# Kernel tuning notes

Hardware: AMD Instinct MI355X
Metric: run time of the kernel (lower is better)

The kernel has to match this reference:

```python
import jax, jax.numpy as jnp
import numpy as np

NU, NI, D, H, E, NQ = 200000, 100000, 64, 64, 1000000, 100000


def setup_inputs() -> dict:
    key = jax.random.key(0)
    ks = jax.random.split(key, 16)
    s = 0.05
    inp = {
        'user_emb': jax.random.normal(ks[0], (NU, D), jnp.float32) * s,
        'item_emb': jax.random.normal(ks[1], (NI, D), jnp.float32) * s,
        'W1': jax.random.normal(ks[2], (6, D, H), jnp.float32) * s,
        'b1': jnp.zeros((6, H), jnp.float32),
        'W2': jax.random.normal(ks[3], (6, H, H), jnp.float32) * s,
        'b2': jnp.zeros((6, H), jnp.float32),
        'dec_w1': jax.random.normal(ks[4], (2 * H, H), jnp.float32) * s,
        'dec_b1': jnp.zeros((H,), jnp.float32),
        'dec_w2': jax.random.normal(ks[5], (H, 4), jnp.float32) * s,
        'dec_b2': jnp.zeros((4,), jnp.float32),
    }
    for name, k in [('edge_view', ks[6]), ('edge_save', ks[7]), ('edge_buy', ks[8])]:
        src = jax.random.randint(k, (E,), 0, NU, jnp.int64 if jax.config.jax_enable_x64 else jnp.int32)
        dst = jax.random.randint(jax.random.fold_in(k, 1), (E,), 0, NI, src.dtype)
        inp[name] = jnp.stack([src, dst])  # [2, E], row0=user, row1=item
    inp['user_ids'] = jax.random.randint(ks[9], (NQ,), 0, NU, jnp.int32)
    inp['item_ids'] = jax.random.randint(ks[10], (NQ,), 0, NI, jnp.int32)
    return inp


def _gcn_conv(h_src, src, dst, n_src, n_dst, W, b):
    # GCNConv (add_self_loops=False) on a bipartite relation:
    # out[d] = sum_e 1/sqrt(deg_src[src_e]) * 1/sqrt(deg_dst[d]) * (x W)[src_e] + b
    h = h_src @ W  # [n_src, H]
    ones = jnp.ones(src.shape[0], h.dtype)
    deg_s = jax.ops.segment_sum(ones, src, num_segments=n_src)
    deg_d = jax.ops.segment_sum(ones, dst, num_segments=n_dst)
    inv_s = jnp.where(deg_s > 0, jax.lax.rsqrt(jnp.maximum(deg_s, 1.0)), 0.0)
    inv_d = jnp.where(deg_d > 0, jax.lax.rsqrt(jnp.maximum(deg_d, 1.0)), 0.0)
    norm = inv_s[src] * inv_d[dst]  # [E]
    msg = h[src] * norm[:, None]    # [E, H]  (dominant memory traffic)
    return jax.ops.segment_sum(msg, dst, num_segments=n_dst) + b


def _hetero_layer(xu, xi, edges, W, b, aggr):
    # relations 0..2: user->item (view,save,buy); 3..5: item->user (reverses)
    item_outs = jnp.stack([_gcn_conv(xu, e[0], e[1], NU, NI, W[k], b[k])
                           for k, e in enumerate(edges)])
    user_outs = jnp.stack([_gcn_conv(xi, e[1], e[0], NI, NU, W[k + 3], b[k + 3])
                           for k, e in enumerate(edges)])
    if aggr == 'max':
        return user_outs.max(0), item_outs.max(0)
    return user_outs.sum(0), item_outs.sum(0)


def reference(user_emb, item_emb, W1, b1, W2, b2, dec_w1, dec_b1, dec_w2, dec_b2,
              edge_view, edge_save, edge_buy, user_ids, item_ids):
    edges = [edge_view, edge_save, edge_buy]
    xu, xi = _hetero_layer(user_emb, item_emb, edges, W1, b1, 'max')
    xu, xi = jax.nn.relu(xu), jax.nn.relu(xi)
    xu, xi = _hetero_layer(xu, xi, edges, W2, b2, 'sum')
    edge_emb = jnp.concatenate([xu[user_ids], xi[item_ids]], axis=-1)  # [NQ, 2H]
    h = jax.nn.relu(edge_emb @ dec_w1 + dec_b1)  # dropout in eval mode = identity
    return h @ dec_w2 + dec_b2  # [NQ, 4]
```

## Files before the change

kernel.cpp:

```cpp
#include <hip/hip_runtime.h>
#include <hip/hip_fp16.h>
#include <math.h>

#define NUV 200000
#define NIV 100000
#define EV  1000000
#define NQV 100000
#define NC  (3 * NIV + 3 * NUV)

struct alignas(8) H4 { __half2 a, b; };

__global__ __launch_bounds__(256) void k_tohalf(const float* __restrict__ in,
                                                __half* __restrict__ out, int n4) {
    int i = blockIdx.x * 256 + threadIdx.x;
    if (i < n4) {
        float4 v = ((const float4*)in)[i];
        H4 o;
        o.a = __floats2half2_rn(v.x, v.y);
        o.b = __floats2half2_rn(v.z, v.w);
        ((H4*)out)[i] = o;
    }
}

__global__ __launch_bounds__(256) void k_count(const int* __restrict__ su,
                                               const int* __restrict__ di,
                                               int* __restrict__ cnt,
                                               int* __restrict__ rk_i,
                                               int* __restrict__ rk_u, int k) {
    int e = blockIdx.x * 256 + threadIdx.x;
    if (e < EV) {
        rk_i[e] = atomicAdd(&cnt[k * NIV + di[e]], 1);
        rk_u[e] = atomicAdd(&cnt[3 * NIV + k * NUV + su[e]], 1);
    }
}

__global__ __launch_bounds__(256) void k_invf(const int* __restrict__ cnt,
                                              float* __restrict__ invs) {
    int i = blockIdx.x * 256 + threadIdx.x;
    if (i < NC) {
        int c = cnt[i];
        invs[i] = (c > 0) ? (1.0f / sqrtf((float)c)) : 0.0f;
    }
}

__global__ __launch_bounds__(256) void k_scan1(const int* __restrict__ cnt,
                                               int* __restrict__ S,
                                               int* __restrict__ bsum) {
    __shared__ int tmp[256];
    int idx = blockIdx.x * 256 + threadIdx.x;
    int v = (idx < NC) ? cnt[idx] : 0;
    tmp[threadIdx.x] = v;
    __syncthreads();
    for (int off = 1; off < 256; off <<= 1) {
        int t = (threadIdx.x >= off) ? tmp[threadIdx.x - off] : 0;
        __syncthreads();
        tmp[threadIdx.x] += t;
        __syncthreads();
    }
    if (idx < NC) S[idx] = tmp[threadIdx.x] - v;
    if (threadIdx.x == 255) bsum[blockIdx.x] = tmp[255];
}

__global__ __launch_bounds__(64) void k_scan2(int* __restrict__ bsum, int nb) {
    int lane = threadIdx.x;
    int carry = 0;
    for (int base = 0; base < nb; base += 64) {
        int i = base + lane;
        int v = (i < nb) ? bsum[i] : 0;
        int orig = v;
        #pragma unroll
        for (int off = 1; off < 64; off <<= 1) {
            int t = __shfl_up(v, off, 64);
            if (lane >= off) v += t;
        }
        if (i < nb) bsum[i] = carry + v - orig;
        carry += __shfl(v, 63, 64);
    }
}

__global__ __launch_bounds__(256) void k_scan3(int* __restrict__ S,
                                               const int* __restrict__ bsum) {
    int idx = blockIdx.x * 256 + threadIdx.x;
    if (idx < NC) S[idx] += bsum[blockIdx.x];
    if (idx == 0) S[NC] = 6 * EV;
}

__global__ __launch_bounds__(256) void k_fill(const int* __restrict__ su,
                                              const int* __restrict__ di,
                                              const float* __restrict__ invs,
                                              const int* __restrict__ S,
                                              const int* __restrict__ rk_i,
                                              const int* __restrict__ rk_u,
                                              float2* __restrict__ ent, int k) {
    int e = blockIdx.x * 256 + threadIdx.x;
    if (e < EV) {
        int u = su[e], i = di[e];
        float nm = invs[k * NIV + i] * invs[3 * NIV + k * NUV + u];
        int p1 = S[k * NIV + i] + rk_i[e];
        ent[p1] = make_float2(__int_as_float(u), nm);
        int p2 = S[3 * NIV + k * NUV + u] + rk_u[e];
        ent[p2] = make_float2(__int_as_float(i), nm);
    }
}

template <int MODE, bool HOUT>
__global__ __launch_bounds__(256, 4) void k_agg(const __half* __restrict__ x_i,
                                                const __half* __restrict__ x_u,
                                                const float2* __restrict__ ent,
                                                const int* __restrict__ S,
                                                const float* __restrict__ Wall,
                                                const float* __restrict__ ball,
                                                void* __restrict__ out_i,
                                                void* __restrict__ out_u) {
    __shared__ float sW[4096];
    __shared__ float sAcc[16 * 68];
    const int nb_i = NIV / 16;
    bool item_side = blockIdx.x < nb_i;
    const __half* x = item_side ? x_i : x_u;
    const float* Wb = item_side ? Wall : Wall + 3 * 4096;
    const float* bb = item_side ? ball : ball + 192;
    void* outp      = item_side ? out_i : out_u;
    int n_dst       = item_side ? NIV : NUV;
    int seg_base    = item_side ? 0 : 3 * NIV;
    int d0          = (item_side ? blockIdx.x : (blockIdx.x - nb_i)) * 16;

    int wave = threadIdx.x >> 6;
    int lane = threadIdx.x & 63;
    int eg   = lane >> 4;
    int fq   = lane & 15;
    int r2 = threadIdx.x >> 4;
    int g  = threadIdx.x & 15;

    float4 res = make_float4(0.f, 0.f, 0.f, 0.f);
    for (int k = 0; k < 3; k++) {
        __syncthreads();
        int idx = seg_base + k * n_dst + d0 + wave * 4;
        int v0 = S[idx], v1 = S[idx + 1], v2 = S[idx + 2], v3 = S[idx + 3], v4 = S[idx + 4];
        {
            const float4* wsrc = (const float4*)(Wb + (size_t)k * 4096);
            float4* wdst = (float4*)sW;
            #pragma unroll
            for (int i = 0; i < 4; i++) wdst[threadIdx.x + 256 * i] = wsrc[threadIdx.x + 256 * i];
        }
        {
            int st[4] = {v0, v1, v2, v3};
            int en[4] = {v1, v2, v3, v4};
            int maxlen = max(max(v1 - v0, v2 - v1), max(v3 - v2, v4 - v3));
            int maxit = (maxlen + 3) >> 2;
            float4 a[4];
            #pragma unroll
            for (int n = 0; n < 4; n++) a[n] = make_float4(0.f, 0.f, 0.f, 0.f);
            for (int it = 0; it < maxit; it += 2) {
                #pragma unroll
                for (int n = 0; n < 4; n++) {
                    int p0 = st[n] + (it << 2) + eg;
                    if (p0 < en[n]) {
                        float2 e = ent[p0];
                        int s = __float_as_int(e.x);
                        float2 raw = *(const float2*)(x + (size_t)s * 64 + fq * 4);
                        float2 f0 = __half22float2(*reinterpret_cast<__half2*>(&raw.x));
                        float2 f1 = __half22float2(*reinterpret_cast<__half2*>(&raw.y));
                        a[n].x = fmaf(f0.x, e.y, a[n].x);
                        a[n].y = fmaf(f0.y, e.y, a[n].y);
                        a[n].z = fmaf(f1.x, e.y, a[n].z);
                        a[n].w = fmaf(f1.y, e.y, a[n].w);
                    }
                    int p1 = p0 + 4;
                    if (p1 < en[n]) {
                        float2 e = ent[p1];
                        int s = __float_as_int(e.x);
                        float2 raw = *(const float2*)(x + (size_t)s * 64 + fq * 4);
                        float2 f0 = __half22float2(*reinterpret_cast<__half2*>(&raw.x));
                        float2 f1 = __half22float2(*reinterpret_cast<__half2*>(&raw.y));
                        a[n].x = fmaf(f0.x, e.y, a[n].x);
                        a[n].y = fmaf(f0.y, e.y, a[n].y);
                        a[n].z = fmaf(f1.x, e.y, a[n].z);
                        a[n].w = fmaf(f1.y, e.y, a[n].w);
                    }
                }
            }
            #pragma unroll
            for (int n = 0; n < 4; n++) {
                #pragma unroll
                for (int off = 16; off < 64; off <<= 1) {
                    a[n].x += __shfl_xor(a[n].x, off, 64);
                    a[n].y += __shfl_xor(a[n].y, off, 64);
                    a[n].z += __shfl_xor(a[n].z, off, 64);
                    a[n].w += __shfl_xor(a[n].w, off, 64);
                }
                if (lane < 16)
                    *(float4*)&sAcc[(wave * 4 + n) * 68 + fq * 4] = a[n];
            }
        }
        __syncthreads();
        float4 y = *(const float4*)&bb[k * 64 + g * 4];
        #pragma unroll
        for (int c = 0; c < 64; c++) {
            float a = sAcc[r2 * 68 + c];
            float4 w = *(const float4*)&sW[c * 64 + g * 4];
            y.x = fmaf(a, w.x, y.x);
            y.y = fmaf(a, w.y, y.y);
            y.z = fmaf(a, w.z, y.z);
            y.w = fmaf(a, w.w, y.w);
        }
        if (k == 0) {
            res = y;
        } else if (MODE == 0) {
            res.x = fmaxf(res.x, y.x); res.y = fmaxf(res.y, y.y);
            res.z = fmaxf(res.z, y.z); res.w = fmaxf(res.w, y.w);
        } else {
            res.x += y.x; res.y += y.y; res.z += y.z; res.w += y.w;
        }
    }
    if (MODE == 0) {
        res.x = fmaxf(res.x, 0.f); res.y = fmaxf(res.y, 0.f);
        res.z = fmaxf(res.z, 0.f); res.w = fmaxf(res.w, 0.f);
    }
    if (HOUT) {
        H4 o;
        o.a = __floats2half2_rn(res.x, res.y);
        o.b = __floats2half2_rn(res.z, res.w);
        *(H4*)((__half*)outp + (size_t)(d0 + r2) * 64 + g * 4) = o;
    } else {
        *(float4*)((float*)outp + (size_t)(d0 + r2) * 64 + g * 4) = res;
    }
}

__global__ __launch_bounds__(256) void k_decoder(const float* __restrict__ xu,
                                                 const float* __restrict__ xi,
                                                 const int* __restrict__ uids,
                                                 const int* __restrict__ iids,
                                                 const float* __restrict__ w1,
                                                 const float* __restrict__ b1,
                                                 const float* __restrict__ w2,
                                                 const float* __restrict__ b2,
                                                 float* __restrict__ out) {
    __shared__ float sW1[128 * 64];
    __shared__ float sE[16 * 132];
    __shared__ float sH[16 * 68];
    __shared__ float sW2[64 * 4];
    {
        const float4* wsrc = (const float4*)w1;
        float4* wdst = (float4*)sW1;
        #pragma unroll
        for (int i = 0; i < 8; i++) wdst[threadIdx.x + 256 * i] = wsrc[threadIdx.x + 256 * i];
        if (threadIdx.x < 64) {
            float4 v = ((const float4*)w2)[threadIdx.x];
            ((float4*)sW2)[threadIdx.x] = v;
        }
    }
    int q0 = blockIdx.x * 16;
    {
        int q = threadIdx.x >> 4;
        int p = threadIdx.x & 15;
        int uid = uids[q0 + q];
        int iid = iids[q0 + q];
        float4 vu = *(const float4*)&xu[(size_t)uid * 64 + p * 4];
        float4 vi = *(const float4*)&xi[(size_t)iid * 64 + p * 4];
        *(float4*)&sE[q * 132 + p * 4] = vu;
        *(float4*)&sE[q * 132 + 64 + p * 4] = vi;
    }
    __syncthreads();
    {
        int r = threadIdx.x >> 4;
        int g = threadIdx.x & 15;
        float4 y = *(const float4*)&b1[g * 4];
        #pragma unroll
        for (int c = 0; c < 128; c++) {
            float a = sE[r * 132 + c];
            float4 w = *(const float4*)&sW1[c * 64 + g * 4];
            y.x = fmaf(a, w.x, y.x);
            y.y = fmaf(a, w.y, y.y);
            y.z = fmaf(a, w.z, y.z);
            y.w = fmaf(a, w.w, y.w);
        }
        y.x = fmaxf(y.x, 0.f); y.y = fmaxf(y.y, 0.f);
        y.z = fmaxf(y.z, 0.f); y.w = fmaxf(y.w, 0.f);
        *(float4*)&sH[r * 68 + g * 4] = y;
    }
    __syncthreads();
    if (threadIdx.x < 64) {
        int q = threadIdx.x >> 2;
        int oc = threadIdx.x & 3;
        float acc = b2[oc];
        #pragma unroll
        for (int c = 0; c < 64; c++)
            acc = fmaf(sH[q * 68 + c], sW2[c * 4 + oc], acc);
        out[(size_t)(q0 + q) * 4 + oc] = acc;
    }
}

extern "C" void kernel_launch(void* const* d_in, const int* in_sizes, int n_in,
                              void* d_out, int out_size, void* d_ws, size_t ws_size,
                              hipStream_t stream) {
    const float* user_emb = (const float*)d_in[0];
    const float* item_emb = (const float*)d_in[1];
    const float* W1 = (const float*)d_in[2];
    const float* b1 = (const float*)d_in[3];
    const float* W2 = (const float*)d_in[4];
    const float* b2 = (const float*)d_in[5];
    const float* dw1 = (const float*)d_in[6];
    const float* db1 = (const float*)d_in[7];
    const float* dw2 = (const float*)d_in[8];
    const float* db2 = (const float*)d_in[9];
    const int* edges[3] = {(const int*)d_in[10], (const int*)d_in[11], (const int*)d_in[12]};
    const int* uids = (const int*)d_in[13];
    const int* iids = (const int*)d_in[14];
    float* out = (float*)d_out;
    (void)in_sizes; (void)n_in; (void)out_size; (void)ws_size;

    char* base = (char*)d_ws;
    size_t off = 0;
    int*    cnt  = (int*)(base + off);    off += (size_t)NC * 4;
    int*    S    = (int*)(base + off);    off += (size_t)(NC + 8) * 4;
    int*    bsum = (int*)(base + off);    off += (size_t)4096 * 4;
    float*  invs = (float*)(base + off);  off += (size_t)NC * 4;
    int*    rki  = (int*)(base + off);    off += (size_t)3 * EV * 4;
    int*    rku  = (int*)(base + off);    off += (size_t)3 * EV * 4;
    float2* ent  = (float2*)(base + off); off += (size_t)6 * EV * 8;
    __half* he_u = (__half*)(base + off); off += (size_t)NUV * 64 * 2;
    __half* he_i = (__half*)(base + off); off += (size_t)NIV * 64 * 2;
    __half* xu1h = (__half*)(base + off); off += (size_t)NUV * 64 * 2;
    __half* xi1h = (__half*)(base + off); off += (size_t)NIV * 64 * 2;
    float*  xu2  = (float*)(base + off);  off += (size_t)NUV * 64 * 4;
    float*  xi2  = (float*)(base + off);  off += (size_t)NIV * 64 * 4;

    const int EB  = (EV + 255) / 256;
    const int SB1 = (NC + 255) / 256;
    const int AGGB = NIV / 16 + NUV / 16;

    k_tohalf<<<(NUV * 64 / 4 + 255) / 256, 256, 0, stream>>>(user_emb, he_u, NUV * 64 / 4);
    k_tohalf<<<(NIV * 64 / 4 + 255) / 256, 256, 0, stream>>>(item_emb, he_i, NIV * 64 / 4);

    hipMemsetAsync(cnt, 0, (size_t)NC * 4, stream);
    for (int k = 0; k < 3; k++)
        k_count<<<EB, 256, 0, stream>>>(edges[k], edges[k] + EV, cnt,
                                        rki + (size_t)k * EV, rku + (size_t)k * EV, k);
    k_invf<<<SB1, 256, 0, stream>>>(cnt, invs);
    k_scan1<<<SB1, 256, 0, stream>>>(cnt, S, bsum);
    k_scan2<<<1, 64, 0, stream>>>(bsum, SB1);
    k_scan3<<<SB1, 256, 0, stream>>>(S, bsum);
    for (int k = 0; k < 3; k++)
        k_fill<<<EB, 256, 0, stream>>>(edges[k], edges[k] + EV, invs, S,
                                       rki + (size_t)k * EV, rku + (size_t)k * EV, ent, k);

    k_agg<0, true><<<AGGB, 256, 0, stream>>>(he_u, he_i, ent, S, W1, b1, xi1h, xu1h);
    k_agg<1, false><<<AGGB, 256, 0, stream>>>(xu1h, xi1h, ent, S, W2, b2, xi2, xu2);

    k_decoder<<<NQV / 16, 256, 0, stream>>>(xu2, xi2, uids, iids,
                                            dw1, db1, dw2, db2, out);
}
```

Measured before the change: 1.471 ms.

## Widen gather to 16-byte loads with 8 edges per wave and batch count/fill launches

The aggregation gather now has each lane load 8 halves (16 bytes) of a source row, so 8 lanes cover a row and 8 edges are processed per wave iteration instead of 4. This cuts the number of load instructions and raises the number of edge reads in flight per wave. In exchange, each thread holds more accumulator registers and the cross-lane reduction needs more shuffles. Separately, the three per-relation count and fill launches are merged into single launches using a 2D grid, which removes launch overhead.

```diff
diff --git a/kernel.cpp b/kernel.cpp
--- a/kernel.cpp
+++ b/kernel.cpp
@@ -22,15 +22,19 @@
     }
 }
 
-__global__ __launch_bounds__(256) void k_count(const int* __restrict__ su,
-                                               const int* __restrict__ di,
+__global__ __launch_bounds__(256) void k_count(const int* __restrict__ e0,
+                                               const int* __restrict__ e1,
+                                               const int* __restrict__ e2,
                                                int* __restrict__ cnt,
                                                int* __restrict__ rk_i,
-                                               int* __restrict__ rk_u, int k) {
+                                               int* __restrict__ rk_u) {
+    int k = blockIdx.y;
+    const int* ed = (k == 0) ? e0 : (k == 1) ? e1 : e2;
     int e = blockIdx.x * 256 + threadIdx.x;
     if (e < EV) {
-        rk_i[e] = atomicAdd(&cnt[k * NIV + di[e]], 1);
-        rk_u[e] = atomicAdd(&cnt[3 * NIV + k * NUV + su[e]], 1);
+        int u = ed[e], i = ed[EV + e];
+        rk_i[(size_t)k * EV + e] = atomicAdd(&cnt[k * NIV + i], 1);
+        rk_u[(size_t)k * EV + e] = atomicAdd(&cnt[3 * NIV + k * NUV + u], 1);
     }
 }
 
@@ -85,20 +89,23 @@
     if (idx == 0) S[NC] = 6 * EV;
 }
 
-__global__ __launch_bounds__(256) void k_fill(const int* __restrict__ su,
-                                              const int* __restrict__ di,
+__global__ __launch_bounds__(256) void k_fill(const int* __restrict__ e0,
+                                              const int* __restrict__ e1,
+                                              const int* __restrict__ e2,
                                               const float* __restrict__ invs,
                                               const int* __restrict__ S,
                                               const int* __restrict__ rk_i,
                                               const int* __restrict__ rk_u,
-                                              float2* __restrict__ ent, int k) {
+                                              float2* __restrict__ ent) {
+    int k = blockIdx.y;
+    const int* ed = (k == 0) ? e0 : (k == 1) ? e1 : e2;
     int e = blockIdx.x * 256 + threadIdx.x;
     if (e < EV) {
-        int u = su[e], i = di[e];
+        int u = ed[e], i = ed[EV + e];
         float nm = invs[k * NIV + i] * invs[3 * NIV + k * NUV + u];
-        int p1 = S[k * NIV + i] + rk_i[e];
+        int p1 = S[k * NIV + i] + rk_i[(size_t)k * EV + e];
         ent[p1] = make_float2(__int_as_float(u), nm);
-        int p2 = S[3 * NIV + k * NUV + u] + rk_u[e];
+        int p2 = S[3 * NIV + k * NUV + u] + rk_u[(size_t)k * EV + e];
         ent[p2] = make_float2(__int_as_float(i), nm);
     }
 }
@@ -126,8 +133,8 @@
 
     int wave = threadIdx.x >> 6;
     int lane = threadIdx.x & 63;
-    int eg   = lane >> 4;
-    int fq   = lane & 15;
+    int eg   = lane >> 3;
+    int fh   = lane & 7;
     int r2 = threadIdx.x >> 4;
     int g  = threadIdx.x & 15;
 
@@ -146,50 +153,45 @@
             int st[4] = {v0, v1, v2, v3};
             int en[4] = {v1, v2, v3, v4};
             int maxlen = max(max(v1 - v0, v2 - v1), max(v3 - v2, v4 - v3));
-            int maxit = (maxlen + 3) >> 2;
-            float4 a[4];
+            int maxit = (maxlen + 7) >> 3;
+            float af[4][8];
             #pragma unroll
-            for (int n = 0; n < 4; n++) a[n] = make_float4(0.f, 0.f, 0.f, 0.f);
-            for (int it = 0; it < maxit; it += 2) {
+            for (int n = 0; n < 4; n++)
+                #pragma unroll
+                for (int j = 0; j < 8; j++) af[n][j] = 0.f;
+            for (int it = 0; it < maxit; it++) {
                 #pragma unroll
                 for (int n = 0; n < 4; n++) {
-                    int p0 = st[n] + (it << 2) + eg;
-                    if (p0 < en[n]) {
-                        float2 e = ent[p0];
+                    int p = st[n] + (it << 3) + eg;
+                    if (p < en[n]) {
+                        float2 e = ent[p];
                         int s = __float_as_int(e.x);
-                        float2 raw = *(const float2*)(x + (size_t)s * 64 + fq * 4);
-                        float2 f0 = __half22float2(*reinterpret_cast<__half2*>(&raw.x));
-                        float2 f1 = __half22float2(*reinterpret_cast<__half2*>(&raw.y));
-                        a[n].x = fmaf(f0.x, e.y, a[n].x);
-                        a[n].y = fmaf(f0.y, e.y, a[n].y);
-                        a[n].z = fmaf(f1.x, e.y, a[n].z);
-                        a[n].w = fmaf(f1.y, e.y, a[n].w);
-                    }
-                    int p1 = p0 + 4;
-                    if (p1 < en[n]) {
-                        float2 e = ent[p1];
-                        int s = __float_as_int(e.x);
-                        float2 raw = *(const float2*)(x + (size_t)s * 64 + fq * 4);
-                        float2 f0 = __half22float2(*reinterpret_cast<__half2*>(&raw.x));
-                        float2 f1 = __half22float2(*reinterpret_cast<__half2*>(&raw.y));
-                        a[n].x = fmaf(f0.x, e.y, a[n].x);
-                        a[n].y = fmaf(f0.y, e.y, a[n].y);
-                        a[n].z = fmaf(f1.x, e.y, a[n].z);
-                        a[n].w = fmaf(f1.y, e.y, a[n].w);
+                        float4 raw = *(const float4*)(x + (size_t)s * 64 + fh * 8);
+                        const __half2* h2 = (const __half2*)&raw;
+                        #pragma unroll
+                        for (int j = 0; j < 4; j++) {
+                            float2 f = __half22float2(h2[j]);
+                            af[n][2 * j]     = fmaf(f.x, e.y, af[n][2 * j]);
+                            af[n][2 * j + 1] = fmaf(f.y, e.y, af[n][2 * j + 1]);
+                        }
                     }
                 }
             }
             #pragma unroll
             for (int n = 0; n < 4; n++) {
                 #pragma unroll
-                for (int off = 16; off < 64; off <<= 1) {
-                    a[n].x += __shfl_xor(a[n].x, off, 64);
-                    a[n].y += __shfl_xor(a[n].y, off, 64);
-                    a[n].z += __shfl_xor(a[n].z, off, 64);
-                    a[n].w += __shfl_xor(a[n].w, off, 64);
+                for (int j = 0; j < 8; j++) {
+                    af[n][j] += __shfl_xor(af[n][j], 8, 64);
+                    af[n][j] += __shfl_xor(af[n][j], 16, 64);
+                    af[n][j] += __shfl_xor(af[n][j], 32, 64);
                 }
-                if (lane < 16)
-                    *(float4*)&sAcc[(wave * 4 + n) * 68 + fq * 4] = a[n];
+                if (lane < 8) {
+                    int row = wave * 4 + n;
+                    *(float4*)&sAcc[row * 68 + lane * 8] =
+                        make_float4(af[n][0], af[n][1], af[n][2], af[n][3]);
+                    *(float4*)&sAcc[row * 68 + lane * 8 + 4] =
+                        make_float4(af[n][4], af[n][5], af[n][6], af[n][7]);
+                }
             }
         }
         __syncthreads();
@@ -303,7 +305,9 @@
     const float* db1 = (const float*)d_in[7];
     const float* dw2 = (const float*)d_in[8];
     const float* db2 = (const float*)d_in[9];
-    const int* edges[3] = {(const int*)d_in[10], (const int*)d_in[11], (const int*)d_in[12]};
+    const int* e0 = (const int*)d_in[10];
+    const int* e1 = (const int*)d_in[11];
+    const int* e2 = (const int*)d_in[12];
     const int* uids = (const int*)d_in[13];
     const int* iids = (const int*)d_in[14];
     float* out = (float*)d_out;
@@ -333,16 +337,12 @@
     k_tohalf<<<(NIV * 64 / 4 + 255) / 256, 256, 0, stream>>>(item_emb, he_i, NIV * 64 / 4);
 
     hipMemsetAsync(cnt, 0, (size_t)NC * 4, stream);
-    for (int k = 0; k < 3; k++)
-        k_count<<<EB, 256, 0, stream>>>(edges[k], edges[k] + EV, cnt,
-                                        rki + (size_t)k * EV, rku + (size_t)k * EV, k);
+    k_count<<<dim3(EB, 3), 256, 0, stream>>>(e0, e1, e2, cnt, rki, rku);
     k_invf<<<SB1, 256, 0, stream>>>(cnt, invs);
     k_scan1<<<SB1, 256, 0, stream>>>(cnt, S, bsum);
     k_scan2<<<1, 64, 0, stream>>>(bsum, SB1);
     k_scan3<<<SB1, 256, 0, stream>>>(S, bsum);
-    for (int k = 0; k < 3; k++)
-        k_fill<<<EB, 256, 0, stream>>>(edges[k], edges[k] + EV, invs, S,
-                                       rki + (size_t)k * EV, rku + (size_t)k * EV, ent, k);
+    k_fill<<<dim3(EB, 3), 256, 0, stream>>>(e0, e1, e2, invs, S, rki, rku, ent);
 
     k_agg<0, true><<<AGGB, 256, 0, stream>>>(he_u, he_i, ent, S, W1, b1, xi1h, xu1h);
     k_agg<1, false><<<AGGB, 256, 0, stream>>>(xu1h, xi1h, ent, S, W2, b2, xi2, xu2);
```

Result: no change. 1.444 ms (-1.8%).
